# Kernel optimization log

Hardware: AMD Instinct MI355X
Metric: run time of the kernel (lower is better)

## Reference

```python
import jax, jax.numpy as jnp
import numpy as np


def setup_inputs() -> dict:
    key = jax.random.key(0)
    ks = jax.random.split(key, 5)
    B, S, H, F, E = 2, 2048, 768, 1536, 8
    scale_h = 1.0 / np.sqrt(H)
    scale_f = 1.0 / np.sqrt(F)
    return {
        "hidden_states": jax.random.normal(ks[0], (B, S, H), dtype=jnp.float32),
        "gate_w": jax.random.normal(ks[1], (E, H), dtype=jnp.float32) * scale_h,
        "w1": jax.random.normal(ks[2], (E, F, H), dtype=jnp.float32) * scale_h,
        "w3": jax.random.normal(ks[3], (E, F, H), dtype=jnp.float32) * scale_h,
        "w2": jax.random.normal(ks[4], (E, H, F), dtype=jnp.float32) * scale_f,
        "k": 2,
    }


def reference(hidden_states, gate_w, w1, w3, w2, k):
    B, S, H = hidden_states.shape
    E = gate_w.shape[0]
    x = hidden_states.reshape(-1, H)                     # [T, H]
    T = x.shape[0]

    # Router: softmax in fp32, top-k, renormalize among selected experts.
    router_logits = x @ gate_w.T                         # [T, E]
    probs = jax.nn.softmax(router_logits.astype(jnp.float32), axis=-1)
    top_w, top_i = jax.lax.top_k(probs, k)               # [T, k]
    top_w = top_w / jnp.sum(top_w, axis=-1, keepdims=True)
    top_w = top_w.astype(x.dtype)

    # Scatter top-k weights into dense [T, E] combine weights (0 for unselected).
    combine = jnp.zeros((T, E), dtype=x.dtype)
    combine = combine.at[jnp.arange(T)[:, None], top_i].set(top_w)

    # SwiGLU experts (zero-weight experts contribute exactly 0 to the sum).
    g = jnp.einsum("th,efh->tef", x, w1)                 # [T, E, F]
    u = jnp.einsum("th,efh->tef", x, w3)                 # [T, E, F]
    act = jax.nn.silu(g) * u                             # [T, E, F]
    expert_out = jnp.einsum("tef,ehf->teh", act, w2)     # [T, E, H]
    y = jnp.einsum("te,teh->th", combine, expert_out)    # [T, H]

    return y.reshape(B, S, H), router_logits
```

## Files before the change

### kernel.cpp

```cpp
#include <hip/hip_runtime.h>
#include <hip/hip_bf16.h>

#define T_TOK 4096
#define H_DIM 768
#define E_NUM 8
#define F_DIM 1536
#define WELEM (E_NUM * F_DIM * H_DIM)

typedef __bf16 bf16x8 __attribute__((ext_vector_type(8)));
typedef float f32x4 __attribute__((ext_vector_type(4)));
typedef unsigned int u32;

#define VMCNT(n) asm volatile("s_waitcnt vmcnt(" #n ")" ::: "memory")
#define CFENCE() asm volatile("" ::: "memory")

__device__ __forceinline__ unsigned short f2bf(float f) {
    unsigned int u = __float_as_uint(f);
    u += 0x7FFF + ((u >> 16) & 1);
    return (unsigned short)(u >> 16);
}

__device__ __forceinline__ float bf2f(unsigned short s) {
    unsigned int u = ((unsigned int)s) << 16;
    return __uint_as_float(u);
}

__device__ __forceinline__ void gload16(const unsigned short* g, unsigned short* l) {
    __builtin_amdgcn_global_load_lds(
        (const __attribute__((address_space(1))) u32*)(g),
        (__attribute__((address_space(3))) u32*)(l),
        16, 0, 0);
}

__global__ __launch_bounds__(256) void prologue_kernel(
    const float* __restrict__ x,
    const float* __restrict__ gw,
    const float* __restrict__ w1,
    const float* __restrict__ w3,
    const float* __restrict__ w2,
    float* __restrict__ logits_out,
    float* __restrict__ weight,
    int* __restrict__ eidx,
    unsigned short* __restrict__ xb,
    unsigned short* __restrict__ w1b,
    unsigned short* __restrict__ w3b,
    unsigned short* __restrict__ w2b) {
    int tid = threadIdx.x;
    if (blockIdx.x >= 1024) {
        int cb = blockIdx.x - 1024;
        int i = (cb * 256 + tid) * 4;
        int stride = (gridDim.x - 1024) * 256 * 4;
        for (; i < 3 * WELEM; i += stride) {
            int r = i / WELEM;
            int j = i - r * WELEM;
            const float* s = (r == 0) ? w1 : (r == 1) ? w3 : w2;
            unsigned short* d = (r == 0) ? w1b : (r == 1) ? w3b : w2b;
            float4 v = *reinterpret_cast<const float4*>(s + j);
            ushort4 o;
            o.x = f2bf(v.x); o.y = f2bf(v.y); o.z = f2bf(v.z); o.w = f2bf(v.w);
            *reinterpret_cast<ushort4*>(d + j) = o;
        }
        return;
    }
    int t = blockIdx.x * 4 + (tid >> 6);
    int lane = tid & 63;

    const float4* xr = reinterpret_cast<const float4*>(x + (size_t)t * H_DIM);
    float4 xv[3];
#pragma unroll
    for (int i = 0; i < 3; ++i) xv[i] = xr[i * 64 + lane];

    unsigned short* xbr = xb + (size_t)t * H_DIM;
#pragma unroll
    for (int i = 0; i < 3; ++i) {
        ushort4 o;
        o.x = f2bf(xv[i].x); o.y = f2bf(xv[i].y);
        o.z = f2bf(xv[i].z); o.w = f2bf(xv[i].w);
        *reinterpret_cast<ushort4*>(xbr + (i * 64 + lane) * 4) = o;
    }

    float v[E_NUM];
#pragma unroll
    for (int e = 0; e < E_NUM; ++e) {
        const float4* g = reinterpret_cast<const float4*>(gw + e * H_DIM);
        float p = 0.f;
#pragma unroll
        for (int i = 0; i < 3; ++i) {
            float4 gv = g[i * 64 + lane];
            p += xv[i].x * gv.x + xv[i].y * gv.y + xv[i].z * gv.z + xv[i].w * gv.w;
        }
        v[e] = p;
    }
#pragma unroll
    for (int d = 1; d < 8; d <<= 1)
#pragma unroll
        for (int e = 0; e < E_NUM; ++e) v[e] += __shfl_xor(v[e], d);
    int me = lane & 7;
    float le = v[0];
#pragma unroll
    for (int e = 1; e < E_NUM; ++e) le = (me == e) ? v[e] : le;
#pragma unroll
    for (int d = 8; d < 64; d <<= 1) le += __shfl_xor(le, d);

    if (lane < 8) logits_out[t * E_NUM + lane] = le;

    float m0 = le;
#pragma unroll
    for (int d = 1; d < 8; d <<= 1) m0 = fmaxf(m0, __shfl_xor(m0, d));
    unsigned long long b0 = __ballot(le == m0);
    int e0 = (__ffsll((long long)b0) - 1) & 7;
    float le1 = (me == e0) ? -3.4e38f : le;
    float m1 = le1;
#pragma unroll
    for (int d = 1; d < 8; d <<= 1) m1 = fmaxf(m1, __shfl_xor(m1, d));
    unsigned long long b1 = __ballot(le1 == m1);
    int e1 = (__ffsll((long long)b1) - 1) & 7;

    if (lane == 0) {
        float w0 = 1.f / (1.f + __expf(m1 - m0));
        weight[t * 2 + 0] = w0;
        weight[t * 2 + 1] = 1.f - w0;
        eidx[t] = e0 | (e1 << 8);
    }
}

__global__ __launch_bounds__(256) void build_lists_kernel(
    const int* __restrict__ eidx,
    int* __restrict__ list,
    int* __restrict__ counts) {
    int e = blockIdx.x;
    int tid = threadIdx.x;
    int lane = tid & 63;
    int wv = tid >> 6;
    __shared__ int wsum[4];
    __shared__ int wbase[4];
    __shared__ int sbase;
    if (tid == 0) sbase = 0;
    __syncthreads();
    for (int c = 0; c < T_TOK; c += 256) {
        int tok = c + tid;
        int pk = eidx[tok];
        int slot = -1;
        if ((pk & 255) == e) slot = tok * 2;
        else if ((pk >> 8) == e) slot = tok * 2 + 1;
        unsigned long long m = __ballot(slot >= 0);
        int prefix = __popcll(m & ((1ull << lane) - 1ull));
        if (lane == 0) wsum[wv] = __popcll(m);
        __syncthreads();
        if (tid == 0) {
            int s = sbase;
#pragma unroll
            for (int i = 0; i < 4; ++i) { wbase[i] = s; s += wsum[i]; }
            sbase = s;
        }
        __syncthreads();
        if (slot >= 0) list[e * T_TOK + wbase[wv] + prefix] = slot;
        __syncthreads();
    }
    if (tid == 0) counts[e] = sbase;
}

__global__ __launch_bounds__(256, 3) void gemm13_kernel(
    const unsigned short* __restrict__ xb,
    const unsigned short* __restrict__ w1b,
    const unsigned short* __restrict__ w3b,
    const int* __restrict__ list,
    const int* __restrict__ counts,
    unsigned short* __restrict__ act) {
    int orig = blockIdx.x;
    int wg = (orig & 7) * 768 + (orig >> 3);
    int tm = wg & 31;
    int tn = (wg >> 5) % 24;
    int e = wg / (32 * 24);

    int cnt = counts[e];
    if (tm * 128 >= cnt) return;
    const int* lst = list + e * T_TOK + tm * 128;
    int mrem = cnt - tm * 128;

    __shared__ unsigned short sA[3][128 * 32];
    __shared__ unsigned short sB1[3][64 * 32];
    __shared__ unsigned short sB3[3][64 * 32];

    int tid = threadIdx.x;
    int lane = tid & 63;
    int wid = tid >> 6;

    int r0 = tid >> 2;
    int r1 = r0 + 64;
    int c8 = ((tid & 3) ^ ((r0 >> 1) & 3)) * 8;
    int tok0 = lst[(r0 < mrem) ? r0 : 0] >> 1;
    int tok1 = lst[(r1 < mrem) ? r1 : 0] >> 1;
    const unsigned short* gA0 = xb + (size_t)tok0 * H_DIM + c8;
    const unsigned short* gA1 = xb + (size_t)tok1 * H_DIM + c8;
    const unsigned short* gB1 = w1b + ((size_t)e * F_DIM + tn * 64 + r0) * H_DIM + c8;
    const unsigned short* gB3 = w3b + ((size_t)e * F_DIM + tn * 64 + r0) * H_DIM + c8;

    auto stage = [&](int b, int kt) {
        gload16(gA0 + kt, &sA[b][wid * 512]);
        gload16(gA1 + kt, &sA[b][2048 + wid * 512]);
        gload16(gB1 + kt, &sB1[b][wid * 512]);
        gload16(gB3 + kt, &sB3[b][wid * 512]);
    };

    int wr = (wid >> 1) * 64;
    int wc = (wid & 1) * 32;
    int fr = lane & 15;
    int kb = ((lane >> 4) ^ ((lane >> 1) & 3)) * 8;

    f32x4 accG[4][2] = {};
    f32x4 accU[4][2] = {};

    const int NT = H_DIM / 32;
    stage(0, 0);
    stage(1, 32);
    int cur = 0;
    for (int t = 0; t < NT; ++t) {
        if (t + 2 < NT) {
            int nb = cur + 2; if (nb >= 3) nb -= 3;
            stage(nb, (t + 2) * 32);
            VMCNT(8);
        } else if (t + 1 < NT) {
            VMCNT(4);
        } else {
            VMCNT(0);
        }
        __builtin_amdgcn_s_barrier();
        CFENCE();

        bf16x8 a[4], b1[2], b3[2];
#pragma unroll
        for (int mi = 0; mi < 4; ++mi)
            a[mi] = *reinterpret_cast<const bf16x8*>(&sA[cur][(wr + mi * 16 + fr) * 32 + kb]);
#pragma unroll
        for (int ni = 0; ni < 2; ++ni) {
            b1[ni] = *reinterpret_cast<const bf16x8*>(&sB1[cur][(wc + ni * 16 + fr) * 32 + kb]);
            b3[ni] = *reinterpret_cast<const bf16x8*>(&sB3[cur][(wc + ni * 16 + fr) * 32 + kb]);
        }
#pragma unroll
        for (int mi = 0; mi < 4; ++mi)
#pragma unroll
            for (int ni = 0; ni < 2; ++ni) {
                accG[mi][ni] = __builtin_amdgcn_mfma_f32_16x16x32_bf16(a[mi], b1[ni], accG[mi][ni], 0, 0, 0);
                accU[mi][ni] = __builtin_amdgcn_mfma_f32_16x16x32_bf16(a[mi], b3[ni], accU[mi][ni], 0, 0, 0);
            }
        CFENCE();
        __builtin_amdgcn_s_barrier();
        cur = (cur + 1 < 3) ? cur + 1 : 0;
    }

    int rg = (lane >> 4) * 4;
    int ci = lane & 15;
#pragma unroll
    for (int mi = 0; mi < 4; ++mi) {
#pragma unroll
        for (int r = 0; r < 4; ++r) {
            int m = wr + mi * 16 + rg + r;
            if (m >= mrem) continue;
            int entry = lst[m];
            size_t rowOff = (size_t)entry * F_DIM + tn * 64;
#pragma unroll
            for (int ni = 0; ni < 2; ++ni) {
                float g = accG[mi][ni][r];
                float u = accU[mi][ni][r];
                float s = g / (1.f + __expf(-g));
                act[rowOff + wc + ni * 16 + ci] = f2bf(s * u);
            }
        }
    }
}

__global__ __launch_bounds__(256, 3) void gemm2_kernel(
    const unsigned short* __restrict__ act,
    const unsigned short* __restrict__ w2b,
    const int* __restrict__ list,
    const int* __restrict__ counts,
    const float* __restrict__ weight,
    unsigned short* __restrict__ ybuf) {
    int orig = blockIdx.x;
    int wg = (orig & 7) * 192 + (orig >> 3);
    int tm = wg & 31;
    int tn = (wg >> 5) % 6;
    int e = wg / (32 * 6);

    int cnt = counts[e];
    if (tm * 128 >= cnt) return;
    const int* lst = list + e * T_TOK + tm * 128;
    int mrem = cnt - tm * 128;

    __shared__ unsigned short sA[3][128 * 32];
    __shared__ unsigned short sB[3][128 * 32];

    int tid = threadIdx.x;
    int lane = tid & 63;
    int wid = tid >> 6;

    int r0 = tid >> 2;
    int r1 = r0 + 64;
    int c8 = ((tid & 3) ^ ((r0 >> 1) & 3)) * 8;
    int row0 = lst[(r0 < mrem) ? r0 : 0];
    int row1 = lst[(r1 < mrem) ? r1 : 0];
    const unsigned short* gA0 = act + (size_t)row0 * F_DIM + c8;
    const unsigned short* gA1 = act + (size_t)row1 * F_DIM + c8;
    const unsigned short* gB0 = w2b + ((size_t)e * H_DIM + tn * 128 + r0) * F_DIM + c8;
    const unsigned short* gB1 = gB0 + (size_t)64 * F_DIM;

    auto stage = [&](int b, int kt) {
        gload16(gA0 + kt, &sA[b][wid * 512]);
        gload16(gA1 + kt, &sA[b][2048 + wid * 512]);
        gload16(gB0 + kt, &sB[b][wid * 512]);
        gload16(gB1 + kt, &sB[b][2048 + wid * 512]);
    };

    int wr = (wid >> 1) * 64;
    int wc = (wid & 1) * 64;
    int fr = lane & 15;
    int kb = ((lane >> 4) ^ ((lane >> 1) & 3)) * 8;

    f32x4 acc[4][4] = {};

    const int NT = F_DIM / 32;
    stage(0, 0);
    stage(1, 32);
    int cur = 0;
    for (int t = 0; t < NT; ++t) {
        if (t + 2 < NT) {
            int nb = cur + 2; if (nb >= 3) nb -= 3;
            stage(nb, (t + 2) * 32);
            VMCNT(8);
        } else if (t + 1 < NT) {
            VMCNT(4);
        } else {
            VMCNT(0);
        }
        __builtin_amdgcn_s_barrier();
        CFENCE();

        bf16x8 a[4], b[4];
#pragma unroll
        for (int mi = 0; mi < 4; ++mi)
            a[mi] = *reinterpret_cast<const bf16x8*>(&sA[cur][(wr + mi * 16 + fr) * 32 + kb]);
#pragma unroll
        for (int ni = 0; ni < 4; ++ni)
            b[ni] = *reinterpret_cast<const bf16x8*>(&sB[cur][(wc + ni * 16 + fr) * 32 + kb]);
#pragma unroll
        for (int mi = 0; mi < 4; ++mi)
#pragma unroll
            for (int ni = 0; ni < 4; ++ni)
                acc[mi][ni] = __builtin_amdgcn_mfma_f32_16x16x32_bf16(a[mi], b[ni], acc[mi][ni], 0, 0, 0);
        CFENCE();
        __builtin_amdgcn_s_barrier();
        cur = (cur + 1 < 3) ? cur + 1 : 0;
    }

    int rg = (lane >> 4) * 4;
    int ci = lane & 15;
#pragma unroll
    for (int mi = 0; mi < 4; ++mi) {
#pragma unroll
        for (int r = 0; r < 4; ++r) {
            int m = wr + mi * 16 + rg + r;
            if (m >= mrem) continue;
            int entry = lst[m];
            float wv = weight[entry];
            size_t rowOff = (size_t)entry * H_DIM + tn * 128;
#pragma unroll
            for (int ni = 0; ni < 4; ++ni)
                ybuf[rowOff + wc + ni * 16 + ci] = f2bf(acc[mi][ni][r] * wv);
        }
    }
}

__global__ __launch_bounds__(256) void combine_kernel(
    const unsigned short* __restrict__ ybuf, float* __restrict__ y) {
    int v = blockIdx.x * blockDim.x + threadIdx.x;
    if (v >= T_TOK * H_DIM / 8) return;
    int t = v / (H_DIM / 8);
    int hv = (v % (H_DIM / 8)) * 8;
    const ushort4* pa = reinterpret_cast<const ushort4*>(ybuf + (size_t)(2 * t) * H_DIM + hv);
    const ushort4* pb = reinterpret_cast<const ushort4*>(ybuf + (size_t)(2 * t + 1) * H_DIM + hv);
    float* yo = y + (size_t)t * H_DIM + hv;
#pragma unroll
    for (int h = 0; h < 2; ++h) {
        ushort4 a = pa[h];
        ushort4 b = pb[h];
        float4 r;
        r.x = bf2f(a.x) + bf2f(b.x);
        r.y = bf2f(a.y) + bf2f(b.y);
        r.z = bf2f(a.z) + bf2f(b.z);
        r.w = bf2f(a.w) + bf2f(b.w);
        *reinterpret_cast<float4*>(yo + h * 4) = r;
    }
}

extern "C" void kernel_launch(void* const* d_in, const int* in_sizes, int n_in,
                              void* d_out, int out_size, void* d_ws, size_t ws_size,
                              hipStream_t stream) {
    const float* x  = (const float*)d_in[0];
    const float* gw = (const float*)d_in[1];
    const float* w1 = (const float*)d_in[2];
    const float* w3 = (const float*)d_in[3];
    const float* w2 = (const float*)d_in[4];

    float* y = (float*)d_out;
    float* logits_out = y + (size_t)T_TOK * H_DIM;

    char* ws = (char*)d_ws;
    size_t off = 0;
    auto alloc = [&](size_t bytes) -> char* {
        char* p = ws + off;
        off += (bytes + 255) & ~(size_t)255;
        return p;
    };
    unsigned short* xb  = (unsigned short*)alloc((size_t)T_TOK * H_DIM * 2);
    unsigned short* w1b = (unsigned short*)alloc((size_t)WELEM * 2);
    unsigned short* w3b = (unsigned short*)alloc((size_t)WELEM * 2);
    unsigned short* w2b = (unsigned short*)alloc((size_t)WELEM * 2);
    unsigned short* act = (unsigned short*)alloc((size_t)T_TOK * 2 * F_DIM * 2);
    unsigned short* ybuf = (unsigned short*)alloc((size_t)T_TOK * 2 * H_DIM * 2);
    float* weight = (float*)alloc((size_t)T_TOK * 2 * 4);
    int* list     = (int*)alloc((size_t)E_NUM * T_TOK * 4);
    int* counts   = (int*)alloc((size_t)E_NUM * 4);
    int* eidx     = (int*)alloc((size_t)T_TOK * 4);

    prologue_kernel<<<4480, 256, 0, stream>>>(x, gw, w1, w3, w2,
                                              logits_out, weight, eidx, xb,
                                              w1b, w3b, w2b);

    build_lists_kernel<<<E_NUM, 256, 0, stream>>>(eidx, list, counts);

    gemm13_kernel<<<6144, 256, 0, stream>>>(xb, w1b, w3b, list, counts, act);

    gemm2_kernel<<<1536, 256, 0, stream>>>(act, w2b, list, counts, weight, ybuf);

    combine_kernel<<<(T_TOK * H_DIM / 8 + 255) / 256, 256, 0, stream>>>(ybuf, y);
}
```

Baseline: 151.2 us.

## Fuse fp32-to-bf16 weight conversion into expert GEMM operand loads

Drops the separate pass that converted all expert weights to bf16 in the prologue. The gate/up and down GEMMs now read fp32 weights straight from global memory into registers, convert them to bf16 and write them to LDS. The async 3-stage LDS pipeline becomes a 2-stage register-prefetch double buffer. This removes a large standalone read/write pass over the weights, but each weight tile is now fetched as fp32 once per token tile, which doubles the bytes read and adds conversion ALU work and register pressure inside the GEMM loops.

```diff
diff --git a/kernel.cpp b/kernel.cpp
--- a/kernel.cpp
+++ b/kernel.cpp
@@ -5,14 +5,11 @@
 #define H_DIM 768
 #define E_NUM 8
 #define F_DIM 1536
-#define WELEM (E_NUM * F_DIM * H_DIM)
 
 typedef __bf16 bf16x8 __attribute__((ext_vector_type(8)));
+typedef unsigned short u16x8 __attribute__((ext_vector_type(8)));
 typedef float f32x4 __attribute__((ext_vector_type(4)));
 typedef unsigned int u32;
-
-#define VMCNT(n) asm volatile("s_waitcnt vmcnt(" #n ")" ::: "memory")
-#define CFENCE() asm volatile("" ::: "memory")
 
 __device__ __forceinline__ unsigned short f2bf(float f) {
     unsigned int u = __float_as_uint(f);
@@ -32,38 +29,15 @@
         16, 0, 0);
 }
 
-__global__ __launch_bounds__(256) void prologue_kernel(
+__global__ __launch_bounds__(256) void router_kernel(
     const float* __restrict__ x,
     const float* __restrict__ gw,
-    const float* __restrict__ w1,
-    const float* __restrict__ w3,
-    const float* __restrict__ w2,
     float* __restrict__ logits_out,
     float* __restrict__ weight,
     int* __restrict__ eidx,
-    unsigned short* __restrict__ xb,
-    unsigned short* __restrict__ w1b,
-    unsigned short* __restrict__ w3b,
-    unsigned short* __restrict__ w2b) {
-    int tid = threadIdx.x;
-    if (blockIdx.x >= 1024) {
-        int cb = blockIdx.x - 1024;
-        int i = (cb * 256 + tid) * 4;
-        int stride = (gridDim.x - 1024) * 256 * 4;
-        for (; i < 3 * WELEM; i += stride) {
-            int r = i / WELEM;
-            int j = i - r * WELEM;
-            const float* s = (r == 0) ? w1 : (r == 1) ? w3 : w2;
-            unsigned short* d = (r == 0) ? w1b : (r == 1) ? w3b : w2b;
-            float4 v = *reinterpret_cast<const float4*>(s + j);
-            ushort4 o;
-            o.x = f2bf(v.x); o.y = f2bf(v.y); o.z = f2bf(v.z); o.w = f2bf(v.w);
-            *reinterpret_cast<ushort4*>(d + j) = o;
-        }
-        return;
-    }
-    int t = blockIdx.x * 4 + (tid >> 6);
-    int lane = tid & 63;
+    unsigned short* __restrict__ xb) {
+    int t = blockIdx.x * 4 + (threadIdx.x >> 6);
+    int lane = threadIdx.x & 63;
 
     const float4* xr = reinterpret_cast<const float4*>(x + (size_t)t * H_DIM);
     float4 xv[3];
@@ -162,8 +136,8 @@
 
 __global__ __launch_bounds__(256, 3) void gemm13_kernel(
     const unsigned short* __restrict__ xb,
-    const unsigned short* __restrict__ w1b,
-    const unsigned short* __restrict__ w3b,
+    const float* __restrict__ w1,
+    const float* __restrict__ w3,
     const int* __restrict__ list,
     const int* __restrict__ counts,
     unsigned short* __restrict__ act) {
@@ -178,9 +152,9 @@
     const int* lst = list + e * T_TOK + tm * 128;
     int mrem = cnt - tm * 128;
 
-    __shared__ unsigned short sA[3][128 * 32];
-    __shared__ unsigned short sB1[3][64 * 32];
-    __shared__ unsigned short sB3[3][64 * 32];
+    __shared__ unsigned short sA[2][128 * 32];
+    __shared__ unsigned short sB1[2][64 * 32];
+    __shared__ unsigned short sB3[2][64 * 32];
 
     int tid = threadIdx.x;
     int lane = tid & 63;
@@ -189,18 +163,22 @@
     int r0 = tid >> 2;
     int r1 = r0 + 64;
     int c8 = ((tid & 3) ^ ((r0 >> 1) & 3)) * 8;
+    int ldsOff = r0 * 32 + (tid & 3) * 8;
     int tok0 = lst[(r0 < mrem) ? r0 : 0] >> 1;
     int tok1 = lst[(r1 < mrem) ? r1 : 0] >> 1;
     const unsigned short* gA0 = xb + (size_t)tok0 * H_DIM + c8;
     const unsigned short* gA1 = xb + (size_t)tok1 * H_DIM + c8;
-    const unsigned short* gB1 = w1b + ((size_t)e * F_DIM + tn * 64 + r0) * H_DIM + c8;
-    const unsigned short* gB3 = w3b + ((size_t)e * F_DIM + tn * 64 + r0) * H_DIM + c8;
-
-    auto stage = [&](int b, int kt) {
-        gload16(gA0 + kt, &sA[b][wid * 512]);
-        gload16(gA1 + kt, &sA[b][2048 + wid * 512]);
-        gload16(gB1 + kt, &sB1[b][wid * 512]);
-        gload16(gB3 + kt, &sB3[b][wid * 512]);
+    const float* gw1 = w1 + ((size_t)e * F_DIM + tn * 64 + r0) * H_DIM + c8;
+    const float* gw3 = w3 + ((size_t)e * F_DIM + tn * 64 + r0) * H_DIM + c8;
+
+    auto writeB = [&](int b, float4 x1a, float4 x1b, float4 x3a, float4 x3b) {
+        u16x8 o1, o3;
+        o1[0] = f2bf(x1a.x); o1[1] = f2bf(x1a.y); o1[2] = f2bf(x1a.z); o1[3] = f2bf(x1a.w);
+        o1[4] = f2bf(x1b.x); o1[5] = f2bf(x1b.y); o1[6] = f2bf(x1b.z); o1[7] = f2bf(x1b.w);
+        o3[0] = f2bf(x3a.x); o3[1] = f2bf(x3a.y); o3[2] = f2bf(x3a.z); o3[3] = f2bf(x3a.w);
+        o3[4] = f2bf(x3b.x); o3[5] = f2bf(x3b.y); o3[6] = f2bf(x3b.z); o3[7] = f2bf(x3b.w);
+        *reinterpret_cast<u16x8*>(&sB1[b][ldsOff]) = o1;
+        *reinterpret_cast<u16x8*>(&sB3[b][ldsOff]) = o3;
     };
 
     int wr = (wid >> 1) * 64;
@@ -212,21 +190,31 @@
     f32x4 accU[4][2] = {};
 
     const int NT = H_DIM / 32;
-    stage(0, 0);
-    stage(1, 32);
+
+    {
+        float4 p1a = *reinterpret_cast<const float4*>(gw1);
+        float4 p1b = *reinterpret_cast<const float4*>(gw1 + 4);
+        float4 p3a = *reinterpret_cast<const float4*>(gw3);
+        float4 p3b = *reinterpret_cast<const float4*>(gw3 + 4);
+        gload16(gA0, &sA[0][wid * 512]);
+        gload16(gA1, &sA[0][2048 + wid * 512]);
+        writeB(0, p1a, p1b, p3a, p3b);
+    }
+    __syncthreads();
+
     int cur = 0;
     for (int t = 0; t < NT; ++t) {
-        if (t + 2 < NT) {
-            int nb = cur + 2; if (nb >= 3) nb -= 3;
-            stage(nb, (t + 2) * 32);
-            VMCNT(8);
-        } else if (t + 1 < NT) {
-            VMCNT(4);
-        } else {
-            VMCNT(0);
-        }
-        __builtin_amdgcn_s_barrier();
-        CFENCE();
+        float4 n1a, n1b, n3a, n3b;
+        bool pre = (t + 1 < NT);
+        if (pre) {
+            int kt = (t + 1) * 32;
+            n1a = *reinterpret_cast<const float4*>(gw1 + kt);
+            n1b = *reinterpret_cast<const float4*>(gw1 + kt + 4);
+            n3a = *reinterpret_cast<const float4*>(gw3 + kt);
+            n3b = *reinterpret_cast<const float4*>(gw3 + kt + 4);
+            gload16(gA0 + kt, &sA[cur ^ 1][wid * 512]);
+            gload16(gA1 + kt, &sA[cur ^ 1][2048 + wid * 512]);
+        }
 
         bf16x8 a[4], b1[2], b3[2];
 #pragma unroll
@@ -244,9 +232,10 @@
                 accG[mi][ni] = __builtin_amdgcn_mfma_f32_16x16x32_bf16(a[mi], b1[ni], accG[mi][ni], 0, 0, 0);
                 accU[mi][ni] = __builtin_amdgcn_mfma_f32_16x16x32_bf16(a[mi], b3[ni], accU[mi][ni], 0, 0, 0);
             }
-        CFENCE();
-        __builtin_amdgcn_s_barrier();
-        cur = (cur + 1 < 3) ? cur + 1 : 0;
+
+        if (pre) writeB(cur ^ 1, n1a, n1b, n3a, n3b);
+        __syncthreads();
+        cur ^= 1;
     }
 
     int rg = (lane >> 4) * 4;
@@ -272,7 +261,7 @@
 
 __global__ __launch_bounds__(256, 3) void gemm2_kernel(
     const unsigned short* __restrict__ act,
-    const unsigned short* __restrict__ w2b,
+    const float* __restrict__ w2,
     const int* __restrict__ list,
     const int* __restrict__ counts,
     const float* __restrict__ weight,
@@ -288,8 +277,8 @@
     const int* lst = list + e * T_TOK + tm * 128;
     int mrem = cnt - tm * 128;
 
-    __shared__ unsigned short sA[3][128 * 32];
-    __shared__ unsigned short sB[3][128 * 32];
+    __shared__ unsigned short sA[2][128 * 32];
+    __shared__ unsigned short sB[2][128 * 32];
 
     int tid = threadIdx.x;
     int lane = tid & 63;
@@ -298,18 +287,22 @@
     int r0 = tid >> 2;
     int r1 = r0 + 64;
     int c8 = ((tid & 3) ^ ((r0 >> 1) & 3)) * 8;
+    int ldsOff = r0 * 32 + (tid & 3) * 8;
     int row0 = lst[(r0 < mrem) ? r0 : 0];
     int row1 = lst[(r1 < mrem) ? r1 : 0];
     const unsigned short* gA0 = act + (size_t)row0 * F_DIM + c8;
     const unsigned short* gA1 = act + (size_t)row1 * F_DIM + c8;
-    const unsigned short* gB0 = w2b + ((size_t)e * H_DIM + tn * 128 + r0) * F_DIM + c8;
-    const unsigned short* gB1 = gB0 + (size_t)64 * F_DIM;
-
-    auto stage = [&](int b, int kt) {
-        gload16(gA0 + kt, &sA[b][wid * 512]);
-        gload16(gA1 + kt, &sA[b][2048 + wid * 512]);
-        gload16(gB0 + kt, &sB[b][wid * 512]);
-        gload16(gB1 + kt, &sB[b][2048 + wid * 512]);
+    const float* gw2a = w2 + ((size_t)e * H_DIM + tn * 128 + r0) * F_DIM + c8;
+    const float* gw2b = gw2a + (size_t)64 * F_DIM;
+
+    auto writeB = [&](int b, float4 xa0, float4 xa1, float4 xb0, float4 xb1) {
+        u16x8 oa, ob;
+        oa[0] = f2bf(xa0.x); oa[1] = f2bf(xa0.y); oa[2] = f2bf(xa0.z); oa[3] = f2bf(xa0.w);
+        oa[4] = f2bf(xa1.x); oa[5] = f2bf(xa1.y); oa[6] = f2bf(xa1.z); oa[7] = f2bf(xa1.w);
+        ob[0] = f2bf(xb0.x); ob[1] = f2bf(xb0.y); ob[2] = f2bf(xb0.z); ob[3] = f2bf(xb0.w);
+        ob[4] = f2bf(xb1.x); ob[5] = f2bf(xb1.y); ob[6] = f2bf(xb1.z); ob[7] = f2bf(xb1.w);
+        *reinterpret_cast<u16x8*>(&sB[b][ldsOff]) = oa;
+        *reinterpret_cast<u16x8*>(&sB[b][2048 + ldsOff]) = ob;
     };
 
     int wr = (wid >> 1) * 64;
@@ -320,21 +313,31 @@
     f32x4 acc[4][4] = {};
 
     const int NT = F_DIM / 32;
-    stage(0, 0);
-    stage(1, 32);
+
+    {
+        float4 pa0 = *reinterpret_cast<const float4*>(gw2a);
+        float4 pa1 = *reinterpret_cast<const float4*>(gw2a + 4);
+        float4 pb0 = *reinterpret_cast<const float4*>(gw2b);
+        float4 pb1 = *reinterpret_cast<const float4*>(gw2b + 4);
+        gload16(gA0, &sA[0][wid * 512]);
+        gload16(gA1, &sA[0][2048 + wid * 512]);
+        writeB(0, pa0, pa1, pb0, pb1);
+    }
+    __syncthreads();
+
     int cur = 0;
     for (int t = 0; t < NT; ++t) {
-        if (t + 2 < NT) {
-            int nb = cur + 2; if (nb >= 3) nb -= 3;
-            stage(nb, (t + 2) * 32);
-            VMCNT(8);
-        } else if (t + 1 < NT) {
-            VMCNT(4);
-        } else {
-            VMCNT(0);
-        }
-        __builtin_amdgcn_s_barrier();
-        CFENCE();
+        float4 na0, na1, nb0, nb1;
+        bool pre = (t + 1 < NT);
+        if (pre) {
+            int kt = (t + 1) * 32;
+            na0 = *reinterpret_cast<const float4*>(gw2a + kt);
+            na1 = *reinterpret_cast<const float4*>(gw2a + kt + 4);
+            nb0 = *reinterpret_cast<const float4*>(gw2b + kt);
+            nb1 = *reinterpret_cast<const float4*>(gw2b + kt + 4);
+            gload16(gA0 + kt, &sA[cur ^ 1][wid * 512]);
+            gload16(gA1 + kt, &sA[cur ^ 1][2048 + wid * 512]);
+        }
 
         bf16x8 a[4], b[4];
 #pragma unroll
@@ -348,9 +351,10 @@
 #pragma unroll
             for (int ni = 0; ni < 4; ++ni)
                 acc[mi][ni] = __builtin_amdgcn_mfma_f32_16x16x32_bf16(a[mi], b[ni], acc[mi][ni], 0, 0, 0);
-        CFENCE();
-        __builtin_amdgcn_s_barrier();
-        cur = (cur + 1 < 3) ? cur + 1 : 0;
+
+        if (pre) writeB(cur ^ 1, na0, na1, nb0, nb1);
+        __syncthreads();
+        cur ^= 1;
     }
 
     int rg = (lane >> 4) * 4;
@@ -412,26 +416,21 @@
         off += (bytes + 255) & ~(size_t)255;
         return p;
     };
-    unsigned short* xb  = (unsigned short*)alloc((size_t)T_TOK * H_DIM * 2);
-    unsigned short* w1b = (unsigned short*)alloc((size_t)WELEM * 2);
-    unsigned short* w3b = (unsigned short*)alloc((size_t)WELEM * 2);
-    unsigned short* w2b = (unsigned short*)alloc((size_t)WELEM * 2);
-    unsigned short* act = (unsigned short*)alloc((size_t)T_TOK * 2 * F_DIM * 2);
+    unsigned short* xb   = (unsigned short*)alloc((size_t)T_TOK * H_DIM * 2);
+    unsigned short* act  = (unsigned short*)alloc((size_t)T_TOK * 2 * F_DIM * 2);
     unsigned short* ybuf = (unsigned short*)alloc((size_t)T_TOK * 2 * H_DIM * 2);
     float* weight = (float*)alloc((size_t)T_TOK * 2 * 4);
     int* list     = (int*)alloc((size_t)E_NUM * T_TOK * 4);
     int* counts   = (int*)alloc((size_t)E_NUM * 4);
     int* eidx     = (int*)alloc((size_t)T_TOK * 4);
 
-    prologue_kernel<<<4480, 256, 0, stream>>>(x, gw, w1, w3, w2,
-                                              logits_out, weight, eidx, xb,
-                                              w1b, w3b, w2b);
+    router_kernel<<<T_TOK / 4, 256, 0, stream>>>(x, gw, logits_out, weight, eidx, xb);
 
     build_lists_kernel<<<E_NUM, 256, 0, stream>>>(eidx, list, counts);
 
-    gemm13_kernel<<<6144, 256, 0, stream>>>(xb, w1b, w3b, list, counts, act);
-
-    gemm2_kernel<<<1536, 256, 0, stream>>>(act, w2b, list, counts, weight, ybuf);
+    gemm13_kernel<<<6144, 256, 0, stream>>>(xb, w1, w3, list, counts, act);
+
+    gemm2_kernel<<<1536, 256, 0, stream>>>(act, w2, list, counts, weight, ybuf);
 
     combine_kernel<<<(T_TOK * H_DIM / 8 + 255) / 256, 256, 0, stream>>>(ybuf, y);
 }
```

Result: slower. 174.1 us (+15.1%).

## Convert w2 to bf16 inside idle gemm13 workgroups instead of prologue

Applied to the files above, without the earlier changes.

Moves the fp32-to-bf16 conversion of w2 out of the prologue kernel and into gemm13 workgroups that have no tokens to process for their expert tile. Each idle workgroup computes a rank among all idle workgroups and converts a strided set of 4096-element chunks. The w2 conversion thus overlaps with the expert GEMM instead of adding serial prologue time, and the prologue grid shrinks. It relies on enough idle tiles existing; all w2 chunks are still covered because the stride equals the total idle count.

```diff
diff --git a/kernel.cpp b/kernel.cpp
--- a/kernel.cpp
+++ b/kernel.cpp
@@ -37,24 +37,22 @@
     const float* __restrict__ gw,
     const float* __restrict__ w1,
     const float* __restrict__ w3,
-    const float* __restrict__ w2,
     float* __restrict__ logits_out,
     float* __restrict__ weight,
     int* __restrict__ eidx,
     unsigned short* __restrict__ xb,
     unsigned short* __restrict__ w1b,
-    unsigned short* __restrict__ w3b,
-    unsigned short* __restrict__ w2b) {
+    unsigned short* __restrict__ w3b) {
     int tid = threadIdx.x;
     if (blockIdx.x >= 1024) {
         int cb = blockIdx.x - 1024;
         int i = (cb * 256 + tid) * 4;
         int stride = (gridDim.x - 1024) * 256 * 4;
-        for (; i < 3 * WELEM; i += stride) {
+        for (; i < 2 * WELEM; i += stride) {
             int r = i / WELEM;
             int j = i - r * WELEM;
-            const float* s = (r == 0) ? w1 : (r == 1) ? w3 : w2;
-            unsigned short* d = (r == 0) ? w1b : (r == 1) ? w3b : w2b;
+            const float* s = (r == 0) ? w1 : w3;
+            unsigned short* d = (r == 0) ? w1b : w3b;
             float4 v = *reinterpret_cast<const float4*>(s + j);
             ushort4 o;
             o.x = f2bf(v.x); o.y = f2bf(v.y); o.z = f2bf(v.z); o.w = f2bf(v.w);
@@ -166,7 +164,9 @@
     const unsigned short* __restrict__ w3b,
     const int* __restrict__ list,
     const int* __restrict__ counts,
-    unsigned short* __restrict__ act) {
+    unsigned short* __restrict__ act,
+    const float* __restrict__ w2,
+    unsigned short* __restrict__ w2b) {
     int orig = blockIdx.x;
     int wg = (orig & 7) * 768 + (orig >> 3);
     int tm = wg & 31;
@@ -174,7 +174,32 @@
     int e = wg / (32 * 24);
 
     int cnt = counts[e];
-    if (tm * 128 >= cnt) return;
+    if (tm * 128 >= cnt) {
+        int acts[E_NUM];
+        int total = 0;
+#pragma unroll
+        for (int k = 0; k < E_NUM; ++k) {
+            int a = (counts[k] + 127) >> 7;
+            acts[k] = a;
+            total += 24 * (32 - a);
+        }
+        int rank = 0;
+#pragma unroll
+        for (int k = 0; k < E_NUM; ++k) if (k < e) rank += 24 * (32 - acts[k]);
+        rank += tn * (32 - acts[e]) + (tm - acts[e]);
+        const int NCHUNK = WELEM / 4096;
+        for (int c = rank; c < NCHUNK; c += total) {
+#pragma unroll
+            for (int pass = 0; pass < 4; ++pass) {
+                int idx = c * 4096 + pass * 1024 + threadIdx.x * 4;
+                float4 v = *reinterpret_cast<const float4*>(w2 + idx);
+                ushort4 o;
+                o.x = f2bf(v.x); o.y = f2bf(v.y); o.z = f2bf(v.z); o.w = f2bf(v.w);
+                *reinterpret_cast<ushort4*>(w2b + idx) = o;
+            }
+        }
+        return;
+    }
     const int* lst = list + e * T_TOK + tm * 128;
     int mrem = cnt - tm * 128;
 
@@ -412,24 +437,24 @@
         off += (bytes + 255) & ~(size_t)255;
         return p;
     };
-    unsigned short* xb  = (unsigned short*)alloc((size_t)T_TOK * H_DIM * 2);
-    unsigned short* w1b = (unsigned short*)alloc((size_t)WELEM * 2);
-    unsigned short* w3b = (unsigned short*)alloc((size_t)WELEM * 2);
-    unsigned short* w2b = (unsigned short*)alloc((size_t)WELEM * 2);
-    unsigned short* act = (unsigned short*)alloc((size_t)T_TOK * 2 * F_DIM * 2);
+    unsigned short* xb   = (unsigned short*)alloc((size_t)T_TOK * H_DIM * 2);
+    unsigned short* w1b  = (unsigned short*)alloc((size_t)WELEM * 2);
+    unsigned short* w3b  = (unsigned short*)alloc((size_t)WELEM * 2);
+    unsigned short* w2b  = (unsigned short*)alloc((size_t)WELEM * 2);
+    unsigned short* act  = (unsigned short*)alloc((size_t)T_TOK * 2 * F_DIM * 2);
     unsigned short* ybuf = (unsigned short*)alloc((size_t)T_TOK * 2 * H_DIM * 2);
     float* weight = (float*)alloc((size_t)T_TOK * 2 * 4);
     int* list     = (int*)alloc((size_t)E_NUM * T_TOK * 4);
     int* counts   = (int*)alloc((size_t)E_NUM * 4);
     int* eidx     = (int*)alloc((size_t)T_TOK * 4);
 
-    prologue_kernel<<<4480, 256, 0, stream>>>(x, gw, w1, w3, w2,
+    prologue_kernel<<<3328, 256, 0, stream>>>(x, gw, w1, w3,
                                               logits_out, weight, eidx, xb,
-                                              w1b, w3b, w2b);
+                                              w1b, w3b);
 
     build_lists_kernel<<<E_NUM, 256, 0, stream>>>(eidx, list, counts);
 
-    gemm13_kernel<<<6144, 256, 0, stream>>>(xb, w1b, w3b, list, counts, act);
+    gemm13_kernel<<<6144, 256, 0, stream>>>(xb, w1b, w3b, list, counts, act, w2, w2b);
 
     gemm2_kernel<<<1536, 256, 0, stream>>>(act, w2b, list, counts, weight, ybuf);
 
```

Result: no change. 153.0 us (+1.2%).
